# Optimization experiments

Hardware: AMD Instinct MI355X
Metric: run time of the kernel (lower is better)

The kernel has to match this reference:

```python
import jax, jax.numpy as jnp
import numpy as np
from jax import lax

EPS = 1e-5  # torch BatchNorm default eps

# Binarization with straight-through estimator (hard-tanh gradient window),
# matching BinaryFunc in dizcza/MCMC_BinaryNet.
@jax.custom_vjp
def binarize(x):
    return jnp.sign(x)

def _bin_fwd(x):
    return jnp.sign(x), x

def _bin_bwd(res, g):
    return (g * (jnp.abs(res) <= 1.0).astype(g.dtype),)

binarize.defvjp(_bin_fwd, _bin_bwd)

def bn2d(x, gamma, beta):
    # training-mode BatchNorm2d: batch stats over (N,H,W), biased variance
    m = x.mean(axis=(0, 2, 3), keepdims=True)
    v = x.var(axis=(0, 2, 3), keepdims=True)
    xn = (x - m) * lax.rsqrt(v + EPS)
    return xn * gamma[None, :, None, None] + beta[None, :, None, None]

def bn1d(x, gamma, beta):
    m = x.mean(axis=0, keepdims=True)
    v = x.var(axis=0, keepdims=True)
    return (x - m) * lax.rsqrt(v + EPS) * gamma[None, :] + beta[None, :]

def bconv(x, w):
    # BinaryDecorator(Conv2d): sign(x) conv sign(W), padding=0, no bias
    return lax.conv_general_dilated(binarize(x), binarize(w), (1, 1), 'VALID',
                                    dimension_numbers=('NCHW', 'OIHW', 'NCHW'))

def maxpool2(x):
    return lax.reduce_window(x, -jnp.inf, lax.max, (1, 1, 2, 2), (1, 1, 2, 2), 'VALID')

def prelu(x, a):
    return jnp.where(x >= 0, x, a * x)


def setup_inputs() -> dict:
    key = jax.random.key(0)
    ks = iter(jax.random.split(key, 16))
    conv_channels = [3, 128, 256, 512]
    fc_sizes = [512 * 6 * 6, 1024, 10]
    d = {'x': jax.random.normal(next(ks), (128, 3, 64, 64), jnp.float32)}
    for i, (cin, cout) in enumerate(zip(conv_channels[:-1], conv_channels[1:])):
        d[f'cg{i}'] = jnp.ones((cin,), jnp.float32)          # BN2d gamma
        d[f'cb{i}'] = jnp.zeros((cin,), jnp.float32)         # BN2d beta
        d[f'cw{i}'] = jax.random.normal(next(ks), (cout, cin, 3, 3), jnp.float32) * 0.05
        d[f'cp{i}'] = jnp.full((1,), 0.25, jnp.float32)      # PReLU (num_parameters=1)
    for i, (fin, fout) in enumerate(zip(fc_sizes[:-1], fc_sizes[1:])):
        d[f'fg{i}'] = jnp.ones((fin,), jnp.float32)
        d[f'fb{i}'] = jnp.zeros((fin,), jnp.float32)
        d[f'fw{i}'] = jax.random.normal(next(ks), (fout, fin), jnp.float32) * 0.05
        d[f'fp{i}'] = jnp.full((1,), 0.25, jnp.float32)
    d['scale'] = jnp.full((1,), 1e-3, jnp.float32)           # ScaleLayer init
    return d


def reference(x, cg0, cb0, cw0, cp0, cg1, cb1, cw1, cp1, cg2, cb2, cw2, cp2,
              fg0, fb0, fw0, fp0, fg1, fb1, fw1, fp1, scale):
    for cg, cb, cw, cp in ((cg0, cb0, cw0, cp0), (cg1, cb1, cw1, cp1), (cg2, cb2, cw2, cp2)):
        x = bn2d(x, cg, cb)
        x = bconv(x, cw)
        x = maxpool2(x)
        x = prelu(x, cp)
    x = x.reshape(x.shape[0], -1)  # [B, 512*6*6]
    for fg, fb, fw, fp in ((fg0, fb0, fw0, fp0), (fg1, fb1, fw1, fp1)):
        x = bn1d(x, fg, fb)
        x = binarize(x) @ binarize(fw).T  # BinaryDecorator(Linear), no bias
        x = prelu(x, fp)
    return x * scale
```

## Files before the change

### kernel.cpp

```cpp
#include <hip/hip_runtime.h>
#include <cstdint>
#include <cstddef>

#define BN_EPS 1e-5


__global__ void zero_d(double* p, int n) {
  int i = blockIdx.x * blockDim.x + threadIdx.x;
  if (i < n) p[i] = 0.0;
}

__global__ void reduce_plane(const float* __restrict__ x, double* __restrict__ sums,
                             int C, int HW) {
  int c = blockIdx.x, n = blockIdx.y;
  const float* p = x + ((long)n * C + c) * HW;
  double s = 0.0, s2 = 0.0;
  for (int i = threadIdx.x; i < HW; i += blockDim.x) {
    double v = (double)p[i];
    s += v; s2 += v * v;
  }
  for (int o = 32; o > 0; o >>= 1) {
    s  += __shfl_down(s, o, 64);
    s2 += __shfl_down(s2, o, 64);
  }
  __shared__ double ls[4], ls2[4];
  int lane = threadIdx.x & 63, w = threadIdx.x >> 6;
  if (lane == 0) { ls[w] = s; ls2[w] = s2; }
  __syncthreads();
  if (threadIdx.x == 0) {
    double a = 0, b = 0;
    for (int i = 0; i < 4; i++) { a += ls[i]; b += ls2[i]; }
    atomicAdd(&sums[2 * c], a);
    atomicAdd(&sums[2 * c + 1], b);
  }
}

__global__ void reduce_cl(const float* __restrict__ x, double* __restrict__ sums,
                          int C, long rows) {
  int lane = threadIdx.x & 63, wv = threadIdx.x >> 6;
  int c = blockIdx.x * 64 + lane;
  double s = 0.0, s2 = 0.0;
  for (long r = blockIdx.y * 4 + wv; r < rows; r += (long)gridDim.y * 4) {
    double v = (double)x[r * C + c];
    s += v; s2 += v * v;
  }
  __shared__ double ls[4][64], ls2[4][64];
  ls[wv][lane] = s; ls2[wv][lane] = s2;
  __syncthreads();
  if (threadIdx.x < 64) {
    double a = ls[0][lane] + ls[1][lane] + ls[2][lane] + ls[3][lane];
    double b = ls2[0][lane] + ls2[1][lane] + ls2[2][lane] + ls2[3][lane];
    atomicAdd(&sums[2 * c], a);
    atomicAdd(&sums[2 * c + 1], b);
  }
}

__global__ void reduce_cols2(const float* __restrict__ x, double* __restrict__ sums,
                             int R, int F, int RS) {
  int f = blockIdx.x * blockDim.x + threadIdx.x;
  int r0 = blockIdx.y * RS, r1 = min(r0 + RS, R);
  double s = 0.0, s2 = 0.0;
  for (int r = r0; r < r1; r++) {
    double v = (double)x[(long)r * F + f];
    s += v; s2 += v * v;
  }
  atomicAdd(&sums[2 * f], s);
  atomicAdd(&sums[2 * f + 1], s2);
}

__global__ void finalize_stats(const double* __restrict__ sums, double2* __restrict__ st,
                               int C, double cnt) {
  int c = blockIdx.x * blockDim.x + threadIdx.x;
  if (c >= C) return;
  double m = sums[2 * c] / cnt;
  double v = sums[2 * c + 1] / cnt - m * m;
  st[c] = make_double2(m, 1.0 / sqrt(v + BN_EPS));
}


__global__ void pack_bits_c1(const float* __restrict__ x, const double2* __restrict__ st,
                             const float* __restrict__ g, const float* __restrict__ b,
                             uint64_t* __restrict__ rows) {
  int wid = blockIdx.x * 4 + (threadIdx.x >> 6);
  int lane = threadIdx.x & 63;
  int n = wid / 192, rem = wid % 192;
  int ci = rem >> 6, y = rem & 63;
  double2 s = st[ci];
  float xv = x[(((long)n * 3 + ci) * 64 + y) * 64 + lane];
  float xn = (float)(((double)xv - s.x) * s.y) * g[ci] + b[ci];
  uint64_t m = __ballot(xn > 0.f);
  if (lane == 0) rows[wid] = m;
}

__global__ void pack_wc1(const float* __restrict__ w, uint32_t* __restrict__ wm) {
  int co = threadIdx.x;
  uint32_t m = 0;
  for (int j = 0; j < 27; j++) m |= (uint32_t)(w[co * 27 + j] > 0.f) << j;
  wm[co] = m;
}

__global__ void pack_cl(const float* __restrict__ acl, const double2* __restrict__ st,
                        const float* __restrict__ g, const float* __restrict__ b,
                        uint64_t* __restrict__ out, int C, long nwords, int lw) {
  long wid = (long)blockIdx.x * 4 + (threadIdx.x >> 6);
  if (wid >= nwords) return;
  int lane = threadIdx.x & 63;
  long row = wid >> lw;
  int w = (int)(wid & ((1 << lw) - 1));
  int c = w * 64 + lane;
  double2 s = st[c];
  float xv = acl[row * C + c];
  float xn = (float)(((double)xv - s.x) * s.y) * g[c] + b[c];
  uint64_t m = __ballot(xn > 0.f);
  if (lane == 0) out[wid] = m;
}

__global__ void pack_wconv(const float* __restrict__ w, uint64_t* __restrict__ out,
                           int CO, int CI, int W) {
  int i = blockIdx.x * blockDim.x + threadIdx.x;
  int total = CO * 9 * W;
  if (i >= total) return;
  int wd = i % W;
  int t = i / W;
  int tap = t % 9, co = t / 9;
  uint64_t bits = 0;
  for (int k = 0; k < 64; k++) {
    int ci = wd * 64 + k;
    bits |= (uint64_t)(w[((long)co * CI + ci) * 9 + tap] > 0.f) << k;
  }
  out[i] = bits;
}

__global__ void pack_nz(const float* __restrict__ x, const double2* __restrict__ st,
                        const float* __restrict__ g, const float* __restrict__ b,
                        uint64_t* __restrict__ out, int R, int F) {
  int Wf = F >> 6;
  long wid = (long)blockIdx.x * 4 + (threadIdx.x >> 6);
  if (wid >= (long)R * Wf) return;
  int lane = threadIdx.x & 63;
  long r = wid / Wf;
  int w = (int)(wid % Wf);
  int f = w * 64 + lane;
  double2 s = st[f];
  double d = (double)x[r * F + f] - s.x;
  float xn = (float)(d * s.y) * g[f] + b[f];
  uint64_t sm = __ballot(xn > 0.f);
  uint64_t nm = __ballot(d != 0.0);
  if (lane == 0) { out[2 * wid] = sm; out[2 * wid + 1] = nm; }
}

__global__ void pack_wfc2(const float* __restrict__ w, uint64_t* __restrict__ out,
                          int O, int F) {
  int Wf = F >> 6;
  long wid = (long)blockIdx.x * 4 + (threadIdx.x >> 6);
  if (wid >= (long)O * Wf) return;
  int lane = threadIdx.x & 63;
  long o = wid / Wf;
  int wd = (int)(wid % Wf);
  uint64_t m = __ballot(w[o * F + wd * 64 + lane] > 0.f);
  if (lane == 0) out[wid] = m;
}


__global__ __launch_bounds__(256) void conv1_pool3(const uint64_t* __restrict__ rows,
                                                   const uint32_t* __restrict__ wm,
                                                   const float* __restrict__ cp,
                                                   float* __restrict__ out) {
  __shared__ uint64_t rL[192];
  __shared__ uint32_t wL[128];
  __shared__ uint32_t mL[61 * 4];
  int n = blockIdx.y, chunk = blockIdx.x, t = threadIdx.x;
  if (t < 192) rL[t] = rows[n * 192 + t];
  if (t < 128) wL[t] = wm[t];
  __syncthreads();
  if (t < 244) {
    int pl = t >> 2, quad = t & 3;
    int pos = chunk * 61 + pl;
    if (pos < 961) {
      int py = pos / 31, px = pos - py * 31;
      int cy = 2 * py + (quad >> 1), cx = 2 * px + (quad & 1);
      uint32_t m = 0;
#pragma unroll
      for (int ci = 0; ci < 3; ci++)
#pragma unroll
        for (int ky = 0; ky < 3; ky++)
          m |= (uint32_t)((rL[ci * 64 + cy + ky] >> cx) & 7) << (ci * 9 + ky * 3);
      mL[pl * 4 + quad] = m;
    }
  }
  __syncthreads();
  int co = t & 127, slot = t >> 7;
  float alpha = cp[0];
  uint32_t w = wL[co];
  for (int i = slot; i < 61; i += 2) {
    int pos = chunk * 61 + i;
    if (pos >= 961) break;
    int p0 = __popc(mL[4 * i] ^ w);
    int p1 = __popc(mL[4 * i + 1] ^ w);
    int p2 = __popc(mL[4 * i + 2] ^ w);
    int p3 = __popc(mL[4 * i + 3] ^ w);
    int dot = 27 - 2 * min(min(p0, p1), min(p2, p3));
    float f = (float)dot;
    out[((long)n * 961 + pos) * 128 + co] = dot >= 0 ? f : alpha * f;
  }
}

template <int W, int IH>
__device__ __forceinline__ void load_half(uint64_t (&h)[4][2 * W],
                                          const uint64_t* __restrict__ sIn,
                                          int py, int cx) {
#pragma unroll
  for (int cy = 0; cy < 4; cy++) {
    const uint64_t* p = &sIn[((2 * py + cy) * IH + cx) * W];
#pragma unroll
    for (int i = 0; i < 2 * W; i++) h[cy][i] = p[i];
  }
}

template <int W>
__device__ __forceinline__ void conv_quad(const uint64_t (&A)[4][2 * W],
                                          const uint64_t (&B)[4][2 * W],
                                          const uint64_t (&wr)[9 * W],
                                          int& a00, int& a01, int& a10, int& a11) {
  a00 = a01 = a10 = a11 = 0;
#pragma unroll
  for (int cy = 0; cy < 4; cy++) {
#pragma unroll
    for (int dy = 0; dy < 2; dy++) {
      int ky = cy - dy;
      if (ky < 0 || ky > 2) continue;
#pragma unroll
      for (int dx = 0; dx < 2; dx++) {
        int acc = 0;
#pragma unroll
        for (int kx = 0; kx < 3; kx++) {
          int col = dx + kx;
#pragma unroll
          for (int wd = 0; wd < W; wd++) {
            uint64_t pv = (col < 2) ? A[cy][col * W + wd] : B[cy][(col - 2) * W + wd];
            acc += __popcll(pv ^ wr[(ky * 3 + kx) * W + wd]);
          }
        }
        if (dy == 0) { if (dx == 0) a00 += acc; else a01 += acc; }
        else         { if (dx == 0) a10 += acc; else a11 += acc; }
      }
    }
  }
}

template <int W, int IH, int PH, int CHUNK>
__global__ __launch_bounds__(256, 4) void convp_slide(
    const uint64_t* __restrict__ in, const uint64_t* __restrict__ wt,
    const float* __restrict__ cp, float* __restrict__ out, int CO) {
  __shared__ uint64_t sIn[IH * IH * W];
  int n = blockIdx.y;
  int cg = blockIdx.x / CHUNK, chunk = blockIdx.x % CHUNK;
  int t = threadIdx.x, lane = t & 63, slot = t >> 6;
  const uint64_t* src = in + (long)n * (IH * IH * W);
  for (int i = t; i < IH * IH * W; i += 256) sIn[i] = src[i];
  int co = cg * 64 + lane;
  uint64_t wr[9 * W];
  const uint64_t* wg = wt + (long)co * (9 * W);
#pragma unroll
  for (int i = 0; i < 9 * W; i++) wr[i] = wg[i];
  __syncthreads();
  int py = chunk * 4 + slot;
  if (py >= PH) return;
  float alpha = cp[0];
  const int K = 9 * 64 * W;
  uint64_t hA[4][2 * W], hB[4][2 * W];
  load_half<W, IH>(hA, sIn, py, 0);
#pragma unroll
  for (int px = 0; px < PH; px += 2) {
    load_half<W, IH>(hB, sIn, py, 2 * px + 2);
    {
      int a00, a01, a10, a11;
      conv_quad<W>(hA, hB, wr, a00, a01, a10, a11);
      int dot = K - 2 * min(min(a00, a01), min(a10, a11));
      float f = (float)dot;
      out[((long)n * PH * PH + py * PH + px) * CO + co] = dot >= 0 ? f : alpha * f;
    }
    if (px + 1 < PH) {
      load_half<W, IH>(hA, sIn, py, 2 * px + 4);
      int a00, a01, a10, a11;
      conv_quad<W>(hB, hA, wr, a00, a01, a10, a11);
      int dot = K - 2 * min(min(a00, a01), min(a10, a11));
      float f = (float)dot;
      out[((long)n * PH * PH + py * PH + px + 1) * CO + co] = dot >= 0 ? f : alpha * f;
    }
  }
}

template <int W, int IH, int PH, int POSCH, bool CL>
__global__ __launch_bounds__(256, 4) void convp_pool3(
    const uint64_t* __restrict__ in, const uint64_t* __restrict__ wt,
    const float* __restrict__ cp, float* __restrict__ out, int CO) {
  __shared__ uint64_t sIn[IH * IH * W];
  int n = blockIdx.y;
  int cg = blockIdx.x / POSCH;
  int chunk = blockIdx.x % POSCH;
  int t = threadIdx.x;
  const uint64_t* src = in + (long)n * (IH * IH * W);
  for (int i = t; i < IH * IH * W; i += 256) sIn[i] = src[i];
  int lane = t & 63;
  int slot = t >> 6;
  int co = cg * 64 + lane;
  uint64_t wr[9 * W];
  const uint64_t* wg = wt + (long)co * (9 * W);
#pragma unroll
  for (int i = 0; i < 9 * W; i++) wr[i] = wg[i];
  __syncthreads();
  float alpha = cp[0];
  for (int pos = chunk * 4 + slot; pos < PH * PH; pos += POSCH * 4) {
    int py = pos / PH, px = pos % PH;
    int a00 = 0, a01 = 0, a10 = 0, a11 = 0;
#pragma unroll
    for (int cy = 0; cy < 4; cy++) {
      uint64_t row[4 * W];
      const uint64_t* rp = &sIn[((2 * py + cy) * IH + 2 * px) * W];
#pragma unroll
      for (int i = 0; i < 4 * W; i++) row[i] = rp[i];
#pragma unroll
      for (int dy = 0; dy < 2; dy++) {
        int ky = cy - dy;
        if (ky < 0 || ky > 2) continue;
#pragma unroll
        for (int dx = 0; dx < 2; dx++) {
          int a = 0;
#pragma unroll
          for (int kx = 0; kx < 3; kx++)
#pragma unroll
            for (int wd = 0; wd < W; wd++)
              a += __popcll(row[(dx + kx) * W + wd] ^ wr[(ky * 3 + kx) * W + wd]);
          if (dy == 0) { if (dx == 0) a00 += a; else a01 += a; }
          else         { if (dx == 0) a10 += a; else a11 += a; }
        }
      }
    }
    int pmin = min(min(a00, a01), min(a10, a11));
    int dot = 9 * 64 * W - 2 * pmin;
    float f = (float)dot;
    long idx = CL ? (((long)n * PH * PH + pos) * CO + co)
                  : (((long)n * CO + co) * PH * PH + pos);
    out[idx] = dot >= 0 ? f : alpha * f;
  }
}


__global__ void fc_bin(const uint64_t* __restrict__ xp, const uint64_t* __restrict__ wp,
                       const float* __restrict__ cp, float* __restrict__ out,
                       int O, int Wf) {
  __shared__ uint64_t xs[288], xz[288];
  int r = blockIdx.y;
  for (int i = threadIdx.x; i < Wf; i += blockDim.x) {
    xs[i] = xp[((long)r * Wf + i) * 2];
    xz[i] = xp[((long)r * Wf + i) * 2 + 1];
  }
  __syncthreads();
  int o = blockIdx.x * blockDim.x + threadIdx.x;
  if (o >= O) return;
  int pc = 0, nzc = 0;
  const uint64_t* wr = wp + (long)o * Wf;
  for (int wd = 0; wd < Wf; wd++) {
    uint64_t nz = xz[wd];
    pc  += __popcll((xs[wd] ^ wr[wd]) & nz);
    nzc += __popcll(nz);
  }
  int dot = nzc - 2 * pc;
  float f = (float)dot;
  float alpha = cp[0];
  out[(long)r * O + o] = dot >= 0 ? f : alpha * f;
}

__global__ void fc_bin_scale(const uint64_t* __restrict__ xp, const uint64_t* __restrict__ wp,
                             const float* __restrict__ cp, const float* __restrict__ scale,
                             float* __restrict__ out, int R, int O, int Wf) {
  int i = blockIdx.x * blockDim.x + threadIdx.x;
  if (i >= R * O) return;
  int o = i % O, r = i / O;
  int pc = 0, nzc = 0;
  for (int wd = 0; wd < Wf; wd++) {
    uint64_t nz = xp[((long)r * Wf + wd) * 2 + 1];
    pc  += __popcll((xp[((long)r * Wf + wd) * 2] ^ wp[(long)o * Wf + wd]) & nz);
    nzc += __popcll(nz);
  }
  int dot = nzc - 2 * pc;
  float f = (float)dot;
  float alpha = cp[0];
  f = dot >= 0 ? f : alpha * f;
  out[i] = f * scale[0];
}


extern "C" void kernel_launch(void* const* d_in, const int* in_sizes, int n_in,
                              void* d_out, int out_size, void* d_ws, size_t ws_size,
                              hipStream_t stream) {
  const float* x   = (const float*)d_in[0];
  const float* cg0 = (const float*)d_in[1];
  const float* cb0 = (const float*)d_in[2];
  const float* cw0 = (const float*)d_in[3];
  const float* cp0 = (const float*)d_in[4];
  const float* cg1 = (const float*)d_in[5];
  const float* cb1 = (const float*)d_in[6];
  const float* cw1 = (const float*)d_in[7];
  const float* cp1 = (const float*)d_in[8];
  const float* cg2 = (const float*)d_in[9];
  const float* cb2 = (const float*)d_in[10];
  const float* cw2 = (const float*)d_in[11];
  const float* cp2 = (const float*)d_in[12];
  const float* fg0 = (const float*)d_in[13];
  const float* fb0 = (const float*)d_in[14];
  const float* fw0 = (const float*)d_in[15];
  const float* fp0 = (const float*)d_in[16];
  const float* fg1 = (const float*)d_in[17];
  const float* fb1 = (const float*)d_in[18];
  const float* fw1 = (const float*)d_in[19];
  const float* fp1 = (const float*)d_in[20];
  const float* scl = (const float*)d_in[21];

  char* ws = (char*)d_ws;
  size_t off = 0;
  auto alloc = [&](size_t bytes) {
    size_t r = off;
    off += (bytes + 255) & ~(size_t)255;
    return r;
  };
  const int C0_OFF = 0, C1_OFF = 16, C2_OFF = 160, C3_OFF = 448, C4_OFF = 18944;
  const int NCH = 19968;

  double*   sums  = (double*)(ws + alloc((size_t)NCH * 2 * sizeof(double)));
  double2*  stats = (double2*)(ws + alloc((size_t)NCH * sizeof(double2)));
  uint64_t* rows0 = (uint64_t*)(ws + alloc(128L * 3 * 64 * 8));
  uint32_t* wm1   = (uint32_t*)(ws + alloc(128L * 4));
  float*    a1    = (float*)(ws + alloc(128L * 961 * 128 * 4));
  uint64_t* s1p   = (uint64_t*)(ws + alloc(128L * 961 * 2 * 8));
  uint64_t* w1p   = (uint64_t*)(ws + alloc(256L * 9 * 2 * 8));
  float*    a2    = (float*)(ws + alloc(128L * 196 * 256 * 4));
  uint64_t* s2p   = (uint64_t*)(ws + alloc(128L * 196 * 4 * 8));
  uint64_t* w2p   = (uint64_t*)(ws + alloc(512L * 9 * 4 * 8));
  float*    a3    = (float*)(ws + alloc(128L * 512 * 36 * 4));
  uint64_t* s3p   = (uint64_t*)(ws + alloc(128L * 288 * 2 * 8));
  uint64_t* w3p   = (uint64_t*)(ws + alloc(1024L * 288 * 8));
  float*    f1    = (float*)(ws + alloc(128L * 1024 * 4));
  uint64_t* s4p   = (uint64_t*)(ws + alloc(128L * 16 * 2 * 8));
  uint64_t* w4p   = (uint64_t*)(ws + alloc(10L * 16 * 8));

  const int B = 256;

  zero_d<<<dim3(156), B, 0, stream>>>(sums, NCH * 2);

  reduce_plane<<<dim3(3, 128), B, 0, stream>>>(x, sums + 2 * C0_OFF, 3, 4096);
  finalize_stats<<<1, 64, 0, stream>>>(sums + 2 * C0_OFF, stats + C0_OFF, 3, 524288.0);
  pack_bits_c1<<<dim3(6144), B, 0, stream>>>(x, stats + C0_OFF, cg0, cb0, rows0);
  pack_wc1<<<1, 128, 0, stream>>>(cw0, wm1);
  conv1_pool3<<<dim3(16, 128), B, 0, stream>>>(rows0, wm1, cp0, a1);

  reduce_cl<<<dim3(2, 256), B, 0, stream>>>(a1, sums + 2 * C1_OFF, 128, 123008L);
  finalize_stats<<<1, 128, 0, stream>>>(sums + 2 * C1_OFF, stats + C1_OFF, 128, 123008.0);
  pack_cl<<<dim3(61504), B, 0, stream>>>(a1, stats + C1_OFF, cg1, cb1, s1p, 128, 246016L, 1);
  pack_wconv<<<dim3(18), B, 0, stream>>>(cw1, w1p, 256, 128, 2);
  convp_slide<2, 31, 14, 4><<<dim3(16, 128), B, 0, stream>>>(s1p, w1p, cp1, a2, 256);

  reduce_cl<<<dim3(4, 128), B, 0, stream>>>(a2, sums + 2 * C2_OFF, 256, 25088L);
  finalize_stats<<<1, 256, 0, stream>>>(sums + 2 * C2_OFF, stats + C2_OFF, 256, 25088.0);
  pack_cl<<<dim3(25088), B, 0, stream>>>(a2, stats + C2_OFF, cg2, cb2, s2p, 256, 100352L, 2);
  pack_wconv<<<dim3(72), B, 0, stream>>>(cw2, w2p, 512, 256, 4);
  convp_pool3<4, 14, 6, 2, false><<<dim3(16, 128), B, 0, stream>>>(s2p, w2p, cp2, a3, 512);

  reduce_cols2<<<dim3(72, 8), B, 0, stream>>>(a3, sums + 2 * C3_OFF, 128, 18432, 16);
  finalize_stats<<<dim3(72), B, 0, stream>>>(sums + 2 * C3_OFF, stats + C3_OFF, 18432, 128.0);
  pack_nz<<<dim3(9216), B, 0, stream>>>(a3, stats + C3_OFF, fg0, fb0, s3p, 128, 18432);
  pack_wfc2<<<dim3(73728), B, 0, stream>>>(fw0, w3p, 1024, 18432);
  fc_bin<<<dim3(4, 128), B, 0, stream>>>(s3p, w3p, fp0, f1, 1024, 288);

  reduce_cols2<<<dim3(4, 8), B, 0, stream>>>(f1, sums + 2 * C4_OFF, 128, 1024, 16);
  finalize_stats<<<dim3(4), B, 0, stream>>>(sums + 2 * C4_OFF, stats + C4_OFF, 1024, 128.0);
  pack_nz<<<dim3(512), B, 0, stream>>>(f1, stats + C4_OFF, fg1, fb1, s4p, 128, 1024);
  pack_wfc2<<<dim3(40), B, 0, stream>>>(fw1, w4p, 10, 1024);
  fc_bin_scale<<<dim3(5), B, 0, stream>>>(s4p, w4p, fp1, scl, (float*)d_out, 128, 10, 16);
}
```

Before: 531.2 us.

## Store conv1 output as int8 with integer BN stats; use sliding conv for layer 3

Conv1 now writes its raw integer dot products as int8 instead of PReLU'd floats. PReLU is folded into BN: the statistics come from integer sums split into positive and negative parts, and the pack kernel applies PReLU on the fly. This cuts the traffic for the largest activation tensor by a factor of four. Layer 3 switches from convp_pool3 to the register-sliding convp_slide kernel, which gains an NCHW output option. Launch bounds drop from 4 to 2 waves per unit, trading occupancy for registers.

```diff
diff --git a/kernel.cpp b/kernel.cpp
--- a/kernel.cpp
+++ b/kernel.cpp
@@ -75,6 +75,67 @@
   double m = sums[2 * c] / cnt;
   double v = sums[2 * c + 1] / cnt - m * m;
   st[c] = make_double2(m, 1.0 / sqrt(v + BN_EPS));
+}
+
+
+__global__ void reduce_a1_i8(const int8_t* __restrict__ a1, int* __restrict__ isums) {
+  __shared__ int ls[128][4];
+  int t = threadIdx.x;
+  if (t < 128) { ls[t][0] = 0; ls[t][1] = 0; ls[t][2] = 0; ls[t][3] = 0; }
+  __syncthreads();
+  int c4 = (t & 31) * 4, slot = t >> 5;
+  int P[4] = {0, 0, 0, 0}, N[4] = {0, 0, 0, 0}, Qp[4] = {0, 0, 0, 0}, Qn[4] = {0, 0, 0, 0};
+  for (long r = (long)blockIdx.x * 8 + slot; r < 123008; r += (long)gridDim.x * 8) {
+    uint32_t u = *(const uint32_t*)(a1 + r * 128 + c4);
+#pragma unroll
+    for (int k = 0; k < 4; k++) {
+      int d = (int)(int8_t)(u >> (8 * k));
+      int dp = max(d, 0), dn = min(d, 0);
+      P[k] += dp; N[k] += dn;
+      Qp[k] += dp * dp; Qn[k] += dn * dn;
+    }
+  }
+#pragma unroll
+  for (int k = 0; k < 4; k++) {
+    int c = c4 + k;
+    atomicAdd(&ls[c][0], P[k]);  atomicAdd(&ls[c][1], N[k]);
+    atomicAdd(&ls[c][2], Qp[k]); atomicAdd(&ls[c][3], Qn[k]);
+  }
+  __syncthreads();
+  if (t < 128) {
+    atomicAdd(&isums[4 * t + 0], ls[t][0]);
+    atomicAdd(&isums[4 * t + 1], ls[t][1]);
+    atomicAdd(&isums[4 * t + 2], ls[t][2]);
+    atomicAdd(&isums[4 * t + 3], ls[t][3]);
+  }
+}
+
+__global__ void finalize_i8(const int* __restrict__ isums, const float* __restrict__ ap,
+                            double2* __restrict__ st, double cnt) {
+  int c = threadIdx.x;
+  double a = (double)ap[0];
+  double sum = (double)isums[4 * c] + a * (double)isums[4 * c + 1];
+  double sq  = (double)isums[4 * c + 2] + a * a * (double)isums[4 * c + 3];
+  double m = sum / cnt;
+  double v = sq / cnt - m * m;
+  st[c] = make_double2(m, 1.0 / sqrt(v + BN_EPS));
+}
+
+__global__ void pack_a1_i8(const int8_t* __restrict__ a1, const double2* __restrict__ st,
+                           const float* __restrict__ g, const float* __restrict__ b,
+                           const float* __restrict__ ap, uint64_t* __restrict__ out) {
+  long wid = (long)blockIdx.x * 4 + (threadIdx.x >> 6);
+  if (wid >= 246016L) return;
+  int lane = threadIdx.x & 63;
+  long row = wid >> 1;
+  int c = (int)((wid & 1) * 64 + lane);
+  float alpha = ap[0];
+  int d = (int)a1[row * 128 + c];
+  float v = d >= 0 ? (float)d : alpha * (float)d;
+  double2 s = st[c];
+  float xn = (float)(((double)v - s.x) * s.y) * g[c] + b[c];
+  uint64_t m = __ballot(xn > 0.f);
+  if (lane == 0) out[wid] = m;
 }
 
 
@@ -164,8 +225,7 @@
 
 __global__ __launch_bounds__(256) void conv1_pool3(const uint64_t* __restrict__ rows,
                                                    const uint32_t* __restrict__ wm,
-                                                   const float* __restrict__ cp,
-                                                   float* __restrict__ out) {
+                                                   int8_t* __restrict__ out) {
   __shared__ uint64_t rL[192];
   __shared__ uint32_t wL[128];
   __shared__ uint32_t mL[61 * 4];
@@ -190,7 +250,6 @@
   }
   __syncthreads();
   int co = t & 127, slot = t >> 7;
-  float alpha = cp[0];
   uint32_t w = wL[co];
   for (int i = slot; i < 61; i += 2) {
     int pos = chunk * 61 + i;
@@ -200,8 +259,7 @@
     int p2 = __popc(mL[4 * i + 2] ^ w);
     int p3 = __popc(mL[4 * i + 3] ^ w);
     int dot = 27 - 2 * min(min(p0, p1), min(p2, p3));
-    float f = (float)dot;
-    out[((long)n * 961 + pos) * 128 + co] = dot >= 0 ? f : alpha * f;
+    out[((long)n * 961 + pos) * 128 + co] = (int8_t)dot;
   }
 }
 
@@ -248,8 +306,8 @@
   }
 }
 
-template <int W, int IH, int PH, int CHUNK>
-__global__ __launch_bounds__(256, 4) void convp_slide(
+template <int W, int IH, int PH, int CHUNK, bool CL>
+__global__ __launch_bounds__(256, 2) void convp_slide(
     const uint64_t* __restrict__ in, const uint64_t* __restrict__ wt,
     const float* __restrict__ cp, float* __restrict__ out, int CO) {
   __shared__ uint64_t sIn[IH * IH * W];
@@ -278,7 +336,9 @@
       conv_quad<W>(hA, hB, wr, a00, a01, a10, a11);
       int dot = K - 2 * min(min(a00, a01), min(a10, a11));
       float f = (float)dot;
-      out[((long)n * PH * PH + py * PH + px) * CO + co] = dot >= 0 ? f : alpha * f;
+      long idx = CL ? (((long)n * PH * PH + py * PH + px) * CO + co)
+                    : (((long)n * CO + co) * PH * PH + py * PH + px);
+      out[idx] = dot >= 0 ? f : alpha * f;
     }
     if (px + 1 < PH) {
       load_half<W, IH>(hA, sIn, py, 2 * px + 4);
@@ -286,63 +346,10 @@
       conv_quad<W>(hB, hA, wr, a00, a01, a10, a11);
       int dot = K - 2 * min(min(a00, a01), min(a10, a11));
       float f = (float)dot;
-      out[((long)n * PH * PH + py * PH + px + 1) * CO + co] = dot >= 0 ? f : alpha * f;
+      long idx = CL ? (((long)n * PH * PH + py * PH + px + 1) * CO + co)
+                    : (((long)n * CO + co) * PH * PH + py * PH + px + 1);
+      out[idx] = dot >= 0 ? f : alpha * f;
     }
-  }
-}
-
-template <int W, int IH, int PH, int POSCH, bool CL>
-__global__ __launch_bounds__(256, 4) void convp_pool3(
-    const uint64_t* __restrict__ in, const uint64_t* __restrict__ wt,
-    const float* __restrict__ cp, float* __restrict__ out, int CO) {
-  __shared__ uint64_t sIn[IH * IH * W];
-  int n = blockIdx.y;
-  int cg = blockIdx.x / POSCH;
-  int chunk = blockIdx.x % POSCH;
-  int t = threadIdx.x;
-  const uint64_t* src = in + (long)n * (IH * IH * W);
-  for (int i = t; i < IH * IH * W; i += 256) sIn[i] = src[i];
-  int lane = t & 63;
-  int slot = t >> 6;
-  int co = cg * 64 + lane;
-  uint64_t wr[9 * W];
-  const uint64_t* wg = wt + (long)co * (9 * W);
-#pragma unroll
-  for (int i = 0; i < 9 * W; i++) wr[i] = wg[i];
-  __syncthreads();
-  float alpha = cp[0];
-  for (int pos = chunk * 4 + slot; pos < PH * PH; pos += POSCH * 4) {
-    int py = pos / PH, px = pos % PH;
-    int a00 = 0, a01 = 0, a10 = 0, a11 = 0;
-#pragma unroll
-    for (int cy = 0; cy < 4; cy++) {
-      uint64_t row[4 * W];
-      const uint64_t* rp = &sIn[((2 * py + cy) * IH + 2 * px) * W];
-#pragma unroll
-      for (int i = 0; i < 4 * W; i++) row[i] = rp[i];
-#pragma unroll
-      for (int dy = 0; dy < 2; dy++) {
-        int ky = cy - dy;
-        if (ky < 0 || ky > 2) continue;
-#pragma unroll
-        for (int dx = 0; dx < 2; dx++) {
-          int a = 0;
-#pragma unroll
-          for (int kx = 0; kx < 3; kx++)
-#pragma unroll
-            for (int wd = 0; wd < W; wd++)
-              a += __popcll(row[(dx + kx) * W + wd] ^ wr[(ky * 3 + kx) * W + wd]);
-          if (dy == 0) { if (dx == 0) a00 += a; else a01 += a; }
-          else         { if (dx == 0) a10 += a; else a11 += a; }
-        }
-      }
-    }
-    int pmin = min(min(a00, a01), min(a10, a11));
-    int dot = 9 * 64 * W - 2 * pmin;
-    float f = (float)dot;
-    long idx = CL ? (((long)n * PH * PH + pos) * CO + co)
-                  : (((long)n * CO + co) * PH * PH + pos);
-    out[idx] = dot >= 0 ? f : alpha * f;
   }
 }
 
@@ -428,11 +435,12 @@
   const int C0_OFF = 0, C1_OFF = 16, C2_OFF = 160, C3_OFF = 448, C4_OFF = 18944;
   const int NCH = 19968;
 
-  double*   sums  = (double*)(ws + alloc((size_t)NCH * 2 * sizeof(double)));
+  double*   sums  = (double*)(ws + alloc(((size_t)NCH * 2 + 256) * sizeof(double)));
+  int*      isums = (int*)(sums + (size_t)NCH * 2);
   double2*  stats = (double2*)(ws + alloc((size_t)NCH * sizeof(double2)));
   uint64_t* rows0 = (uint64_t*)(ws + alloc(128L * 3 * 64 * 8));
   uint32_t* wm1   = (uint32_t*)(ws + alloc(128L * 4));
-  float*    a1    = (float*)(ws + alloc(128L * 961 * 128 * 4));
+  int8_t*   a1    = (int8_t*)(ws + alloc(128L * 961 * 128));
   uint64_t* s1p   = (uint64_t*)(ws + alloc(128L * 961 * 2 * 8));
   uint64_t* w1p   = (uint64_t*)(ws + alloc(256L * 9 * 2 * 8));
   float*    a2    = (float*)(ws + alloc(128L * 196 * 256 * 4));
@@ -447,25 +455,25 @@
 
   const int B = 256;
 
-  zero_d<<<dim3(156), B, 0, stream>>>(sums, NCH * 2);
+  zero_d<<<dim3(157), B, 0, stream>>>(sums, NCH * 2 + 256);
 
   reduce_plane<<<dim3(3, 128), B, 0, stream>>>(x, sums + 2 * C0_OFF, 3, 4096);
   finalize_stats<<<1, 64, 0, stream>>>(sums + 2 * C0_OFF, stats + C0_OFF, 3, 524288.0);
   pack_bits_c1<<<dim3(6144), B, 0, stream>>>(x, stats + C0_OFF, cg0, cb0, rows0);
   pack_wc1<<<1, 128, 0, stream>>>(cw0, wm1);
-  conv1_pool3<<<dim3(16, 128), B, 0, stream>>>(rows0, wm1, cp0, a1);
-
-  reduce_cl<<<dim3(2, 256), B, 0, stream>>>(a1, sums + 2 * C1_OFF, 128, 123008L);
-  finalize_stats<<<1, 128, 0, stream>>>(sums + 2 * C1_OFF, stats + C1_OFF, 128, 123008.0);
-  pack_cl<<<dim3(61504), B, 0, stream>>>(a1, stats + C1_OFF, cg1, cb1, s1p, 128, 246016L, 1);
+  conv1_pool3<<<dim3(16, 128), B, 0, stream>>>(rows0, wm1, a1);
+
+  reduce_a1_i8<<<dim3(96), B, 0, stream>>>(a1, isums);
+  finalize_i8<<<1, 128, 0, stream>>>(isums, cp0, stats + C1_OFF, 123008.0);
+  pack_a1_i8<<<dim3(61504), B, 0, stream>>>(a1, stats + C1_OFF, cg1, cb1, cp0, s1p);
   pack_wconv<<<dim3(18), B, 0, stream>>>(cw1, w1p, 256, 128, 2);
-  convp_slide<2, 31, 14, 4><<<dim3(16, 128), B, 0, stream>>>(s1p, w1p, cp1, a2, 256);
+  convp_slide<2, 31, 14, 4, true><<<dim3(16, 128), B, 0, stream>>>(s1p, w1p, cp1, a2, 256);
 
   reduce_cl<<<dim3(4, 128), B, 0, stream>>>(a2, sums + 2 * C2_OFF, 256, 25088L);
   finalize_stats<<<1, 256, 0, stream>>>(sums + 2 * C2_OFF, stats + C2_OFF, 256, 25088.0);
   pack_cl<<<dim3(25088), B, 0, stream>>>(a2, stats + C2_OFF, cg2, cb2, s2p, 256, 100352L, 2);
   pack_wconv<<<dim3(72), B, 0, stream>>>(cw2, w2p, 512, 256, 4);
-  convp_pool3<4, 14, 6, 2, false><<<dim3(16, 128), B, 0, stream>>>(s2p, w2p, cp2, a3, 512);
+  convp_slide<4, 14, 6, 2, false><<<dim3(16, 128), B, 0, stream>>>(s2p, w2p, cp2, a3, 512);
 
   reduce_cols2<<<dim3(72, 8), B, 0, stream>>>(a3, sums + 2 * C3_OFF, 128, 18432, 16);
   finalize_stats<<<dim3(72), B, 0, stream>>>(sums + 2 * C3_OFF, stats + C3_OFF, 18432, 128.0);
```

Result: slower. 556.9 us (+4.8%).
